# Kernel optimization log

Measured on AMD Instinct MI355X. Metric: run time of the kernel, lower is better.

## Reference

```python
import jax, jax.numpy as jnp
import numpy as np

EPS = 1e-5


def _bn(h, g, b):
    # training-mode batch norm over the point dimension
    m = jnp.mean(h, axis=0)
    v = jnp.mean(jnp.square(h), axis=0) - jnp.square(m)
    return g * (h - m) * jax.lax.rsqrt(v + EPS) + b


def _convtr2(x, w):
    # generative transpose conv, stride 2: each point spawns 8 children. w: [8, Cin, Cout]
    n = x.shape[0]
    return jnp.einsum('nc,kcd->nkd', x, w).reshape(n * 8, w.shape[-1])


def _conv3(x, idx, mask, w):
    # 3^3 stride-1 sparse conv via kernel-map gather + per-offset GEMM, accumulated with scan.
    # idx, mask: [27, N]; w: [27, Cin, Cout]
    acc0 = jnp.zeros((idx.shape[1], w.shape[-1]), x.dtype)

    def step(acc, kin):
        i_k, m_k, w_k = kin
        return acc + (x[i_k] * m_k[:, None]) @ w_k, None

    out, _ = jax.lax.scan(step, acc0, (idx, mask, w))
    return out


def setup_inputs() -> dict:
    key = jax.random.key(0)
    ks = jax.random.split(key, 16)
    N0, N1, N2 = 8000, 64000, 512000
    s = lambda k, shape, fan: jax.random.normal(k, shape, jnp.float32) * (1.0 / np.sqrt(fan))
    return {
        'x': jax.random.normal(ks[0], (N0, 128), jnp.float32),
        'w_tr1': s(ks[1], (8, 128, 96), 128),
        'g1': jnp.ones((96,), jnp.float32), 'b1': jnp.zeros((96,), jnp.float32),
        'idx1': jax.random.randint(ks[2], (27, N1), 0, N1, jnp.int32),
        'mask1': (jax.random.uniform(ks[3], (27, N1)) < 0.7).astype(jnp.float32),
        'w_c1': s(ks[4], (27, 96, 64), 27 * 96),
        'g2': jnp.ones((64,), jnp.float32), 'b2': jnp.zeros((64,), jnp.float32),
        'w_tr2': s(ks[5], (8, 64, 64), 64),
        'g3': jnp.ones((64,), jnp.float32), 'b3': jnp.zeros((64,), jnp.float32),
        'idx2': jax.random.randint(ks[6], (27, N2), 0, N2, jnp.int32),
        'mask2': (jax.random.uniform(ks[7], (27, N2)) < 0.7).astype(jnp.float32),
        'w_c2': s(ks[8], (27, 64, 32), 27 * 64),
        'g4': jnp.ones((32,), jnp.float32), 'b4': jnp.zeros((32,), jnp.float32),
        'w_dec': s(ks[9], (32, 96), 32),
        'g5': jnp.ones((96,), jnp.float32), 'b5': jnp.zeros((96,), jnp.float32),
    }


def reference(x, w_tr1, g1, b1, idx1, mask1, w_c1, g2, b2,
              w_tr2, g3, b3, idx2, mask2, w_c2, g4, b4, w_dec, g5, b5):
    relu = jax.nn.relu
    h = relu(_bn(_convtr2(x, w_tr1), g1, b1))            # [8*N0, 96]
    h = relu(_bn(_conv3(h, idx1, mask1, w_c1), g2, b2))  # [N1, 64]
    h = relu(_bn(_convtr2(h, w_tr2), g3, b3))            # [N2, 64]
    h = relu(_bn(_conv3(h, idx2, mask2, w_c2), g4, b4))  # [N2, 32]
    intensity_res = jnp.mean(h, axis=1, keepdims=True)   # mean_me: feature-dim mean
    remi2seg = relu(_bn(h @ w_dec, g5, b5))              # [N2, 96]
    return intensity_res, remi2seg
```

## Files before the change

kernel.cpp:

```cpp
#include <hip/hip_runtime.h>
#include <hip/hip_bf16.h>


#define EPSF 1e-5f
#define N2 512000

typedef __attribute__((ext_vector_type(8))) short short8v;
typedef __attribute__((ext_vector_type(4))) short short4v;
typedef __attribute__((ext_vector_type(4))) float f32x4;

__device__ __forceinline__ float bf2f(short u) {
  return __uint_as_float(((unsigned int)(unsigned short)u) << 16);
}
__device__ __forceinline__ short f2bf(float f) {
  __hip_bfloat16 h = __float2bfloat16(f);
  return *(short*)&h;
}

__global__ __launch_bounds__(256) void idxprep_k(int* __restrict__ i1,
                                                 const float* __restrict__ m1,
                                                 int n1, int z1,
                                                 int* __restrict__ i2,
                                                 const float* __restrict__ m2,
                                                 int n2, int z2) {
  const int i = blockIdx.x * 256 + threadIdx.x;
  if (i < n1 && m1[i] == 0.f) i1[i] = z1;
  if (i < n2 && m2[i] == 0.f) i2[i] = z2;
}

__global__ __launch_bounds__(256) void wconvA_k(
    const float* __restrict__ wc1, const float* __restrict__ wc2,
    const float* __restrict__ wt1, const float* __restrict__ wt2,
    const float* __restrict__ x,
    ushort* __restrict__ o_wc1, ushort* __restrict__ o_wc2,
    ushort* __restrict__ o_wt1, ushort* __restrict__ o_wt2,
    ushort* __restrict__ o_xb) {
  const int i = blockIdx.x * 256 + threadIdx.x;
  if (i < 165888) {
    int k = i / 6144, r = i % 6144, c = r / 64, d = r % 64;
    o_wc1[(k * 64 + d) * 96 + c] = (ushort)f2bf(wc1[i]);
  } else if (i < 221184) {
    int j = i - 165888;
    int k = j / 2048, r = j % 2048, c = r / 32, d = r % 32;
    o_wc2[(k * 32 + d) * 64 + c] = (ushort)f2bf(wc2[j]);
  } else if (i < 319488) {
    int j = i - 221184;
    int k = j / 12288, r = j % 12288, c = r / 96, d = r % 96;
    o_wt1[(k * 96 + d) * 128 + c] = (ushort)f2bf(wt1[j]);
  } else if (i < 352256) {
    int j = i - 319488;
    int k = j / 4096, r = j % 4096, c = r / 64, d = r % 64;
    o_wt2[(k * 64 + d) * 64 + c] = (ushort)f2bf(wt2[j]);
  } else if (i < 1376256) {
    int j = i - 352256;
    o_xb[j] = (ushort)f2bf(x[j]);
  }
}

__global__ __launch_bounds__(256) void wconvB_k(const float* __restrict__ wdec,
                                                ushort* __restrict__ o_wd) {
  const int i = blockIdx.x * 256 + threadIdx.x;
  if (i < 3072) {
    int c = i / 96, d = i % 96;
    o_wd[d * 32 + c] = (ushort)f2bf(wdec[i]);
  }
}

template <int CIN, int COUT, int NK, int WPB>
__global__ __launch_bounds__(WPB * 64) void convtrm_k(const ushort* __restrict__ xb,
                                                      const ushort* __restrict__ wtb,
                                                      ushort* __restrict__ yb,
                                                      float* __restrict__ st, int N) {
  constexpr int KS = CIN / 32;
  constexpr int NT = COUT / 16;
  const int t = threadIdx.x, wid = t >> 6, lane = t & 63;
  const int r16 = lane & 15, g = lane >> 4, co = g * 8;
  const int base = (blockIdx.x * WPB + wid) * 32;

  short8v A[2][KS];
#pragma unroll
  for (int m = 0; m < 2; ++m) {
    const ushort* rp = xb + (size_t)(base + m * 16 + r16) * CIN + co;
#pragma unroll
    for (int s = 0; s < KS; ++s) A[m][s] = *(const short8v*)(rp + s * 32);
  }
  float s_l[NT], q_l[NT];
#pragma unroll
  for (int n = 0; n < NT; ++n) { s_l[n] = 0.f; q_l[n] = 0.f; }

#pragma unroll 1
  for (int k = 0; k < NK; ++k) {
    f32x4 acc[2][NT];
#pragma unroll
    for (int m = 0; m < 2; ++m)
#pragma unroll
      for (int n = 0; n < NT; ++n) acc[m][n] = (f32x4)0.f;
    const ushort* wb = wtb + ((size_t)k * COUT + r16) * CIN + co;
#pragma unroll
    for (int n = 0; n < NT; ++n)
#pragma unroll
      for (int s = 0; s < KS; ++s) {
        short8v bv = *(const short8v*)(wb + n * 16 * CIN + s * 32);
        acc[0][n] = __builtin_amdgcn_mfma_f32_16x16x32_bf16(A[0][s], bv, acc[0][n], 0, 0, 0);
        acc[1][n] = __builtin_amdgcn_mfma_f32_16x16x32_bf16(A[1][s], bv, acc[1][n], 0, 0, 0);
      }
#pragma unroll
    for (int m = 0; m < 2; ++m)
#pragma unroll
      for (int n = 0; n < NT; ++n)
#pragma unroll
        for (int j = 0; j < 4; ++j) {
          float v = acc[m][n][j];
          yb[((size_t)(base + m * 16 + g * 4 + j) * NK + k) * COUT + n * 16 + r16] =
              (ushort)f2bf(v);
          s_l[n] += v; q_l[n] += v * v;
        }
  }
  __shared__ float sl[2 * COUT];
  for (int i = t; i < 2 * COUT; i += WPB * 64) sl[i] = 0.f;
  __syncthreads();
#pragma unroll
  for (int n = 0; n < NT; ++n) {
    atomicAdd(&sl[n * 16 + r16], s_l[n]);
    atomicAdd(&sl[COUT + n * 16 + r16], q_l[n]);
  }
  __syncthreads();
  for (int i = t; i < 2 * COUT; i += WPB * 64) atomicAdd(&st[i], sl[i]);
}

template <int CIN, int COUT, int MT>
__global__ __launch_bounds__(256) void conv3m2_k(const ushort* __restrict__ hb,
                                                 const int* __restrict__ idxp,
                                                 const ushort* __restrict__ wtb,
                                                 ushort* __restrict__ yb,
                                                 float* __restrict__ st, int N) {
  constexpr int KS = CIN / 32;
  constexpr int NT = COUT / 16;
  constexpr int PPB = 4 * MT * 16;
  __shared__ int lidx[27 * PPB];
  const int t = threadIdx.x, wid = t >> 6, lane = t & 63;
  const int r16 = lane & 15, g = lane >> 4, co = g * 8;
  const int B0 = blockIdx.x * PPB;

  for (int j = t; j < 27 * PPB; j += 256)
    lidx[j] = idxp[(size_t)(j / PPB) * N + B0 + (j % PPB)];
  __syncthreads();

  const int wbase = wid * MT * 16 + r16;

  f32x4 acc[MT][NT];
#pragma unroll
  for (int m = 0; m < MT; ++m)
#pragma unroll
    for (int n = 0; n < NT; ++n) acc[m][n] = (f32x4)0.f;

  short8v A0[MT][KS], A1[MT][KS], A2[MT][KS];
  int i0[MT], i1[MT], i2[MT];

#define LIDX(dst, kk)                                                      \
  { _Pragma("unroll") for (int m = 0; m < MT; ++m)                         \
        dst[m] = lidx[(kk) * PPB + wbase + m * 16]; }

#define GROW(A, ixr)                                                       \
  { _Pragma("unroll") for (int m = 0; m < MT; ++m) {                       \
      const ushort* rp = hb + (size_t)ixr[m] * CIN + co;                   \
      _Pragma("unroll") for (int s = 0; s < KS; ++s)                       \
          A[m][s] = *(const short8v*)(rp + s * 32);                        \
    } }

#define MMA(A, kk)                                                         \
  { const ushort* wb = wtb + ((size_t)(kk) * COUT + r16) * CIN + co;       \
    _Pragma("unroll") for (int n = 0; n < NT; ++n)                         \
        _Pragma("unroll") for (int s = 0; s < KS; ++s) {                   \
      short8v bv = *(const short8v*)(wb + n * 16 * CIN + s * 32);          \
      _Pragma("unroll") for (int m = 0; m < MT; ++m)                       \
          acc[m][n] = __builtin_amdgcn_mfma_f32_16x16x32_bf16(             \
              A[m][s], bv, acc[m][n], 0, 0, 0);                            \
    } }

  LIDX(i0, 0) GROW(A0, i0)
  LIDX(i1, 1) GROW(A1, i1)
  LIDX(i2, 2)
#pragma unroll 1
  for (int j = 0; j < 8; ++j) {
    GROW(A2, i2) LIDX(i0, 3 * j + 3) MMA(A0, 3 * j)
    GROW(A0, i0) LIDX(i1, 3 * j + 4) MMA(A1, 3 * j + 1)
    GROW(A1, i1) LIDX(i2, 3 * j + 5) MMA(A2, 3 * j + 2)
  }
  GROW(A2, i2)
  MMA(A0, 24) MMA(A1, 25) MMA(A2, 26)
#undef LIDX
#undef GROW
#undef MMA

  const int base = B0 + wid * MT * 16;
  float s_l[NT], q_l[NT];
#pragma unroll
  for (int n = 0; n < NT; ++n) { s_l[n] = 0.f; q_l[n] = 0.f; }
#pragma unroll
  for (int m = 0; m < MT; ++m)
#pragma unroll
    for (int n = 0; n < NT; ++n)
#pragma unroll
      for (int j = 0; j < 4; ++j) {
        float v = acc[m][n][j];
        yb[(size_t)(base + m * 16 + g * 4 + j) * COUT + n * 16 + r16] = (ushort)f2bf(v);
        s_l[n] += v; q_l[n] += v * v;
      }
  __shared__ float sl[2 * COUT];
  if (t < 2 * COUT) sl[t] = 0.f;
  __syncthreads();
#pragma unroll
  for (int n = 0; n < NT; ++n) {
    atomicAdd(&sl[n * 16 + r16], s_l[n]);
    atomicAdd(&sl[COUT + n * 16 + r16], q_l[n]);
  }
  __syncthreads();
  if (t < 2 * COUT) atomicAdd(&st[t], sl[t]);
}

template <int C>
__global__ __launch_bounds__(256) void bn_bb_k(const ushort* __restrict__ in,
                                               ushort* __restrict__ out, int N,
                                               const float* __restrict__ st,
                                               const float* __restrict__ g,
                                               const float* __restrict__ b) {
  __shared__ float scs[C], bis[C];
  const int t = threadIdx.x;
  if (t < C) {
    const float invN = 1.f / (float)N;
    float m = st[t] * invN;
    float var = st[C + t] * invN - m * m;
    float rs = rsqrtf(var + EPSF);
    scs[t] = g[t] * rs;
    bis[t] = b[t] - m * g[t] * rs;
  }
  __syncthreads();
  const long total8 = (long)N * C / 8;
  for (long i = (long)blockIdx.x * 256 + t; i < total8; i += (long)gridDim.x * 256) {
    const int c0 = (int)((8 * i) % C);
    short8v v = *(const short8v*)(in + 8 * i);
    short8v o;
#pragma unroll
    for (int j = 0; j < 8; ++j) {
      float f = bf2f(v[j]);
      o[j] = f2bf(fmaxf(0.f, fmaf(f, scs[c0 + j], bis[c0 + j])));
    }
    *(short8v*)(out + 8 * i) = o;
  }
}

__global__ __launch_bounds__(256) void kint2_k(const ushort* __restrict__ y4b,
                                               float* __restrict__ inten,
                                               const float* __restrict__ st4,
                                               const float* __restrict__ g4,
                                               const float* __restrict__ b4,
                                               ushort* __restrict__ h4b) {
  __shared__ float sc[32], bi[32];
  const int t = threadIdx.x;
  if (t < 32) {
    const float invN = 1.f / (float)N2;
    float m = st4[t] * invN;
    float v = st4[32 + t] * invN - m * m;
    float rs = rsqrtf(v + EPSF);
    sc[t] = g4[t] * rs;
    bi[t] = b4[t] - m * g4[t] * rs;
  }
  __syncthreads();
  const int r = blockIdx.x * 256 + t;
  const ushort* yr = y4b + (size_t)r * 32;
  ushort* hr = h4b + (size_t)r * 32;
  float sum = 0.f;
#pragma unroll
  for (int q = 0; q < 4; ++q) {
    short8v v = *(const short8v*)(yr + 8 * q);
    short8v o;
#pragma unroll
    for (int j = 0; j < 8; ++j) {
      int c = 8 * q + j;
      float h = fmaxf(0.f, fmaf(bf2f(v[j]), sc[c], bi[c]));
      sum += h;
      o[j] = f2bf(h);
    }
    *(short8v*)(hr + 8 * q) = o;
  }
  inten[r] = sum * (1.f / 32.f);
}

__global__ __launch_bounds__(256) void kM2_k(const ushort* __restrict__ h4b,
                                             float* __restrict__ Mg,
                                             float* __restrict__ csum) {
  __shared__ float Mb[1024];
  __shared__ float Sb[32];
  const int t = threadIdx.x;
  for (int i = t; i < 1024; i += 256) Mb[i] = 0.f;
  if (t < 32) Sb[t] = 0.f;
  __syncthreads();
  const int wave = t >> 6, lane = t & 63;
  const int ci = (lane >> 3) * 4, cj = (lane & 7) * 4;
  float macc[16];
  float scl[4];
#pragma unroll
  for (int a = 0; a < 16; ++a) macc[a] = 0.f;
#pragma unroll
  for (int a = 0; a < 4; ++a) scl[a] = 0.f;
  const int base = blockIdx.x * 1000 + wave * 250;
  for (int r = 0; r < 250; ++r) {
    const ushort* yr = h4b + (size_t)(base + r) * 32;
    short4v u = *(const short4v*)(yr + ci);
    short4v w = *(const short4v*)(yr + cj);
    float hu[4], hv[4];
#pragma unroll
    for (int a = 0; a < 4; ++a) { hu[a] = bf2f(u[a]); hv[a] = bf2f(w[a]); }
#pragma unroll
    for (int a = 0; a < 4; ++a)
#pragma unroll
      for (int q = 0; q < 4; ++q) macc[a * 4 + q] = fmaf(hu[a], hv[q], macc[a * 4 + q]);
#pragma unroll
    for (int q = 0; q < 4; ++q) scl[q] += hv[q];
  }
#pragma unroll
  for (int a = 0; a < 4; ++a)
#pragma unroll
    for (int q = 0; q < 4; ++q) atomicAdd(&Mb[(ci + a) * 32 + cj + q], macc[a * 4 + q]);
  if ((lane >> 3) == 0) {
#pragma unroll
    for (int q = 0; q < 4; ++q) atomicAdd(&Sb[cj + q], scl[q]);
  }
  __syncthreads();
  for (int i = t; i < 1024; i += 256) atomicAdd(&Mg[i], Mb[i]);
  if (t < 32) atomicAdd(&csum[t], Sb[t]);
}

__global__ __launch_bounds__(128) void kstat5_k(const float* __restrict__ colsum_g,
                                                const float* __restrict__ Mg,
                                                const float* __restrict__ wd,
                                                const float* __restrict__ g5,
                                                const float* __restrict__ b5,
                                                float* __restrict__ sc5g,
                                                float* __restrict__ bi5g) {
  __shared__ float wl[3072], Ml[1024], csl[32];
  const int t = threadIdx.x;
  for (int i = t * 4; i < 3072; i += 512)
    *(float4*)&wl[i] = *(const float4*)&wd[i];
  for (int i = t; i < 1024; i += 128) Ml[i] = Mg[i];
  if (t < 32) csl[t] = colsum_g[t];
  __syncthreads();
  if (t < 96) {
    const float invN = 1.f / (float)N2;
    float mean = 0.f;
#pragma unroll
    for (int c = 0; c < 32; ++c) mean = fmaf(csl[c], wl[c * 96 + t], mean);
    mean *= invN;
    float q = 0.f;
    for (int c1 = 0; c1 < 32; ++c1) {
      float tmp = 0.f;
#pragma unroll
      for (int c2 = 0; c2 < 32; ++c2) tmp = fmaf(Ml[c1 * 32 + c2], wl[c2 * 96 + t], tmp);
      q = fmaf(wl[c1 * 96 + t], tmp, q);
    }
    float var = q * invN - mean * mean;
    float rs = rsqrtf(var + EPSF);
    float sc = g5[t] * rs;
    sc5g[t] = sc;
    bi5g[t] = b5[t] - mean * sc;
  }
}

__global__ __launch_bounds__(256) void kfinal2_k(const ushort* __restrict__ h4b,
                                                 const ushort* __restrict__ wdT,
                                                 const float* __restrict__ sc5g,
                                                 const float* __restrict__ bi5g,
                                                 float* __restrict__ outR) {
  const int t = threadIdx.x, wid = t >> 6, lane = t & 63;
  const int r16 = lane & 15, g = lane >> 4, co = g * 8;
  const int base = (blockIdx.x * 4 + wid) * 32;

  short8v a[2];
#pragma unroll
  for (int m = 0; m < 2; ++m)
    a[m] = *(const short8v*)(h4b + (size_t)(base + m * 16 + r16) * 32 + co);

  f32x4 acc[2][6];
#pragma unroll
  for (int m = 0; m < 2; ++m)
#pragma unroll
    for (int n = 0; n < 6; ++n) acc[m][n] = (f32x4)0.f;
#pragma unroll
  for (int n = 0; n < 6; ++n) {
    short8v bv = *(const short8v*)(wdT + (size_t)(n * 16 + r16) * 32 + co);
    acc[0][n] = __builtin_amdgcn_mfma_f32_16x16x32_bf16(a[0], bv, acc[0][n], 0, 0, 0);
    acc[1][n] = __builtin_amdgcn_mfma_f32_16x16x32_bf16(a[1], bv, acc[1][n], 0, 0, 0);
  }
#pragma unroll
  for (int n = 0; n < 6; ++n) {
    const int col = n * 16 + r16;
    const float sc = sc5g[col], bi = bi5g[col];
#pragma unroll
    for (int m = 0; m < 2; ++m)
#pragma unroll
      for (int j = 0; j < 4; ++j)
        outR[(size_t)(base + m * 16 + g * 4 + j) * 96 + col] =
            fmaxf(0.f, fmaf(acc[m][n][j], sc, bi));
  }
}

extern "C" void kernel_launch(void* const* d_in, const int* in_sizes, int n_in,
                              void* d_out, int out_size, void* d_ws, size_t ws_size,
                              hipStream_t stream) {
  const float* x     = (const float*)d_in[0];
  const float* w_tr1 = (const float*)d_in[1];
  const float* g1    = (const float*)d_in[2];
  const float* b1    = (const float*)d_in[3];
  int*         idx1  = (int*)d_in[4];
  const float* mask1 = (const float*)d_in[5];
  const float* w_c1  = (const float*)d_in[6];
  const float* g2    = (const float*)d_in[7];
  const float* b2    = (const float*)d_in[8];
  const float* w_tr2 = (const float*)d_in[9];
  const float* g3    = (const float*)d_in[10];
  const float* b3    = (const float*)d_in[11];
  int*         idx2  = (int*)d_in[12];
  const float* mask2 = (const float*)d_in[13];
  const float* w_c2  = (const float*)d_in[14];
  const float* g4    = (const float*)d_in[15];
  const float* b4    = (const float*)d_in[16];
  const float* w_dec = (const float*)d_in[17];
  const float* g5    = (const float*)d_in[18];
  const float* b5    = (const float*)d_in[19];

  float* outF  = (float*)d_out;
  float* inten = outF;
  float* R     = outF + 512000;

  ushort* y1b = (ushort*)R;
  ushort* h1b = (ushort*)(R + 3200000);
  ushort* y2b = (ushort*)(R + 6400000);
  ushort* h2b = (ushort*)(R + 8500000);
  ushort* y3b = (ushort*)(R + 16384000);
  ushort* h3b = (ushort*)R;
  ushort* y4b = (ushort*)(R + 32800000);
  ushort* xb  = (ushort*)(R + 41100000);

  float* iw  = inten;
  float* st1 = iw + 0;
  float* st2 = iw + 192;
  float* st3 = iw + 320;
  ushort* w1T  = (ushort*)(iw + 448);
  ushort* w2T  = (ushort*)(iw + 83392);
  ushort* wt1T = (ushort*)(iw + 111040);
  ushort* wt2T = (ushort*)(iw + 160192);

  float* xw   = (float*)d_in[0];
  float* st4  = xw + 0;
  float* csum = xw + 64;
  float* Mg   = xw + 96;
  float* sc5g = xw + 1120;
  float* bi5g = xw + 1216;
  ushort* wdT = (ushort*)(xw + 1312);

  ushort* h4s = (ushort*)d_in[12];

  hipMemsetAsync(st1, 0, 448 * sizeof(float), stream);
  hipMemsetAsync((void*)(R + 6272000), 0, 192, stream);
  idxprep_k<<<54000, 256, 0, stream>>>(idx1, mask1, 27 * 64000, 64000,
                                       idx2, mask2, 27 * N2, N2);
  wconvA_k<<<5376, 256, 0, stream>>>(w_c1, w_c2, w_tr1, w_tr2, x,
                                     w1T, w2T, wt1T, wt2T, xb);
  hipMemsetAsync(st4, 0, 1120 * sizeof(float), stream);
  wconvB_k<<<12, 256, 0, stream>>>(w_dec, wdT);

  convtrm_k<128, 96, 8, 2><<<125, 128, 0, stream>>>(xb, wt1T, y1b, st1, 8000);
  bn_bb_k<96><<<1024, 256, 0, stream>>>(y1b, h1b, 64000, st1, g1, b1);
  conv3m2_k<96, 64, 1><<<1000, 256, 0, stream>>>(h1b, idx1, w1T, y2b, st2, 64000);
  bn_bb_k<64><<<1024, 256, 0, stream>>>(y2b, h2b, 64000, st2, g2, b2);
  convtrm_k<64, 64, 8, 4><<<500, 256, 0, stream>>>(h2b, wt2T, y3b, st3, 64000);
  bn_bb_k<64><<<2048, 256, 0, stream>>>(y3b, h3b, N2, st3, g3, b3);
  hipMemsetAsync((void*)(R + 16384000), 0, 128, stream);
  conv3m2_k<64, 32, 2><<<4000, 256, 0, stream>>>(h3b, idx2, w2T, y4b, st4, N2);

  kint2_k<<<2000, 256, 0, stream>>>(y4b, inten, st4, g4, b4, h4s);
  kM2_k<<<512, 256, 0, stream>>>(h4s, Mg, csum);
  kstat5_k<<<1, 128, 0, stream>>>(csum, Mg, w_dec, g5, b5, sc5g, bi5g);
  kfinal2_k<<<4000, 256, 0, stream>>>(h4s, wdT, sc5g, bi5g, R);
}
```

Baseline: 1.031 ms.

## Fuse mask-to-zero-row index prep into sparse conv and deepen gather pipeline

Drops the separate idxprep kernel that rewrote masked indices in place. The conv kernel now reads idx and mask together while filling its shared index table, substituting the zero row for masked entries. This removes a launch and a read-modify-write pass over both index arrays, in exchange for extra mask reads inside the conv. The gather/MMA software pipeline also goes from three to four register buffers, prefetching further ahead at the cost of more registers.

```diff
diff --git a/kernel.cpp b/kernel.cpp
--- a/kernel.cpp
+++ b/kernel.cpp
@@ -15,17 +15,6 @@
 __device__ __forceinline__ short f2bf(float f) {
   __hip_bfloat16 h = __float2bfloat16(f);
   return *(short*)&h;
-}
-
-__global__ __launch_bounds__(256) void idxprep_k(int* __restrict__ i1,
-                                                 const float* __restrict__ m1,
-                                                 int n1, int z1,
-                                                 int* __restrict__ i2,
-                                                 const float* __restrict__ m2,
-                                                 int n2, int z2) {
-  const int i = blockIdx.x * 256 + threadIdx.x;
-  if (i < n1 && m1[i] == 0.f) i1[i] = z1;
-  if (i < n2 && m2[i] == 0.f) i2[i] = z2;
 }
 
 __global__ __launch_bounds__(256) void wconvA_k(
@@ -129,11 +118,13 @@
 }
 
 template <int CIN, int COUT, int MT>
-__global__ __launch_bounds__(256) void conv3m2_k(const ushort* __restrict__ hb,
-                                                 const int* __restrict__ idxp,
+__global__ __launch_bounds__(256) void conv3m3_k(const ushort* __restrict__ hb,
+                                                 const int* __restrict__ idx,
+                                                 const float* __restrict__ mask,
                                                  const ushort* __restrict__ wtb,
                                                  ushort* __restrict__ yb,
-                                                 float* __restrict__ st, int N) {
+                                                 float* __restrict__ st, int N,
+                                                 int ZR) {
   constexpr int KS = CIN / 32;
   constexpr int NT = COUT / 16;
   constexpr int PPB = 4 * MT * 16;
@@ -142,8 +133,11 @@
   const int r16 = lane & 15, g = lane >> 4, co = g * 8;
   const int B0 = blockIdx.x * PPB;
 
-  for (int j = t; j < 27 * PPB; j += 256)
-    lidx[j] = idxp[(size_t)(j / PPB) * N + B0 + (j % PPB)];
+  for (int j = t; j < 27 * PPB; j += 256) {
+    const size_t off = (size_t)(j / PPB) * N + B0 + (j % PPB);
+    const int iv = idx[off];
+    lidx[j] = (mask[off] != 0.f) ? iv : ZR;
+  }
   __syncthreads();
 
   const int wbase = wid * MT * 16 + r16;
@@ -154,8 +148,8 @@
 #pragma unroll
     for (int n = 0; n < NT; ++n) acc[m][n] = (f32x4)0.f;
 
-  short8v A0[MT][KS], A1[MT][KS], A2[MT][KS];
-  int i0[MT], i1[MT], i2[MT];
+  short8v A0[MT][KS], A1[MT][KS], A2[MT][KS], A3[MT][KS];
+  int i0[MT], i1[MT], i2[MT], i3[MT];
 
 #define LIDX(dst, kk)                                                      \
   { _Pragma("unroll") for (int m = 0; m < MT; ++m)                         \
@@ -180,14 +174,19 @@
 
   LIDX(i0, 0) GROW(A0, i0)
   LIDX(i1, 1) GROW(A1, i1)
-  LIDX(i2, 2)
+  LIDX(i2, 2) GROW(A2, i2)
 #pragma unroll 1
-  for (int j = 0; j < 8; ++j) {
-    GROW(A2, i2) LIDX(i0, 3 * j + 3) MMA(A0, 3 * j)
-    GROW(A0, i0) LIDX(i1, 3 * j + 4) MMA(A1, 3 * j + 1)
-    GROW(A1, i1) LIDX(i2, 3 * j + 5) MMA(A2, 3 * j + 2)
-  }
-  GROW(A2, i2)
+  for (int j4 = 0; j4 < 5; ++j4) {
+    const int k = 4 * j4;
+    LIDX(i3, k + 3) GROW(A3, i3) MMA(A0, k)
+    LIDX(i0, k + 4) GROW(A0, i0) MMA(A1, k + 1)
+    LIDX(i1, k + 5) GROW(A1, i1) MMA(A2, k + 2)
+    LIDX(i2, k + 6) GROW(A2, i2) MMA(A3, k + 3)
+  }
+  LIDX(i3, 23) GROW(A3, i3) MMA(A0, 20)
+  LIDX(i0, 24) GROW(A0, i0) MMA(A1, 21)
+  LIDX(i1, 25) GROW(A1, i1) MMA(A2, 22)
+  LIDX(i2, 26) GROW(A2, i2) MMA(A3, 23)
   MMA(A0, 24) MMA(A1, 25) MMA(A2, 26)
 #undef LIDX
 #undef GROW
@@ -412,7 +411,7 @@
   const float* w_tr1 = (const float*)d_in[1];
   const float* g1    = (const float*)d_in[2];
   const float* b1    = (const float*)d_in[3];
-  int*         idx1  = (int*)d_in[4];
+  const int*   idx1  = (const int*)d_in[4];
   const float* mask1 = (const float*)d_in[5];
   const float* w_c1  = (const float*)d_in[6];
   const float* g2    = (const float*)d_in[7];
@@ -420,7 +419,7 @@
   const float* w_tr2 = (const float*)d_in[9];
   const float* g3    = (const float*)d_in[10];
   const float* b3    = (const float*)d_in[11];
-  int*         idx2  = (int*)d_in[12];
+  const int*   idx2  = (const int*)d_in[12];
   const float* mask2 = (const float*)d_in[13];
   const float* w_c2  = (const float*)d_in[14];
   const float* g4    = (const float*)d_in[15];
@@ -463,8 +462,6 @@
 
   hipMemsetAsync(st1, 0, 448 * sizeof(float), stream);
   hipMemsetAsync((void*)(R + 6272000), 0, 192, stream);
-  idxprep_k<<<54000, 256, 0, stream>>>(idx1, mask1, 27 * 64000, 64000,
-                                       idx2, mask2, 27 * N2, N2);
   wconvA_k<<<5376, 256, 0, stream>>>(w_c1, w_c2, w_tr1, w_tr2, x,
                                      w1T, w2T, wt1T, wt2T, xb);
   hipMemsetAsync(st4, 0, 1120 * sizeof(float), stream);
@@ -472,12 +469,14 @@
 
   convtrm_k<128, 96, 8, 2><<<125, 128, 0, stream>>>(xb, wt1T, y1b, st1, 8000);
   bn_bb_k<96><<<1024, 256, 0, stream>>>(y1b, h1b, 64000, st1, g1, b1);
-  conv3m2_k<96, 64, 1><<<1000, 256, 0, stream>>>(h1b, idx1, w1T, y2b, st2, 64000);
+  conv3m3_k<96, 64, 1><<<1000, 256, 0, stream>>>(h1b, idx1, mask1, w1T, y2b, st2,
+                                                 64000, 64000);
   bn_bb_k<64><<<1024, 256, 0, stream>>>(y2b, h2b, 64000, st2, g2, b2);
   convtrm_k<64, 64, 8, 4><<<500, 256, 0, stream>>>(h2b, wt2T, y3b, st3, 64000);
   bn_bb_k<64><<<2048, 256, 0, stream>>>(y3b, h3b, N2, st3, g3, b3);
   hipMemsetAsync((void*)(R + 16384000), 0, 128, stream);
-  conv3m2_k<64, 32, 2><<<4000, 256, 0, stream>>>(h3b, idx2, w2T, y4b, st4, N2);
+  conv3m3_k<64, 32, 2><<<4000, 256, 0, stream>>>(h3b, idx2, mask2, w2T, y4b, st4,
+                                                 N2, N2);
 
   kint2_k<<<2000, 256, 0, stream>>>(y4b, inten, st4, g4, b4, h4s);
   kM2_k<<<512, 256, 0, stream>>>(h4s, Mg, csum);
```

After: 990.0 us. 1.04x faster.
